# Optimization experiments

Hardware: AMD Instinct MI355X
Metric: run time of the kernel (lower is better)

Reference implementation:

```python
import jax, jax.numpy as jnp
import numpy as np

GRID = 64
N_NODES = GRID * GRID
LN_EPS = 1e-5


def _grid_edge_index(n=GRID):
    ids = np.arange(n * n, dtype=np.int32).reshape(n, n)
    r0, r1 = ids[:, :-1].ravel(), ids[:, 1:].ravel()   # horizontal neighbors
    d0, d1 = ids[:-1, :].ravel(), ids[1:, :].ravel()   # vertical neighbors
    src = np.concatenate([r0, r1, d0, d1])
    dst = np.concatenate([r1, r0, d1, d0])
    return np.stack([src, dst])  # [2, 16128] directed edges


def setup_inputs() -> dict:
    key = jax.random.key(0)
    ks = jax.random.split(key, 6)
    B, C, H, L = 128, 12, 64, 3
    s_in = 1.0 / np.sqrt(C)
    s_h = 1.0 / np.sqrt(H)
    return {
        "x": jax.random.normal(ks[0], (B, C, GRID, GRID), jnp.float32),
        "edge_index": jnp.asarray(_grid_edge_index()),
        "w_in": jax.random.normal(ks[1], (C, H), jnp.float32) * s_in,
        "b_in": jnp.zeros((H,), jnp.float32),
        "w_self": jax.random.normal(ks[2], (L, H, H), jnp.float32) * s_h,
        "w_neigh": jax.random.normal(ks[3], (L, H, H), jnp.float32) * s_h,
        "conv_b": jnp.zeros((L, H), jnp.float32),
        "ln_g": jnp.ones((L, H), jnp.float32),
        "ln_b": jnp.zeros((L, H), jnp.float32),
        "w_head": jax.random.normal(ks[4], (H, 1), jnp.float32) * s_h,
        "b_head": jnp.zeros((1,), jnp.float32),
    }


def reference(x, edge_index, w_in, b_in, w_self, w_neigh, conv_b, ln_g, ln_b, w_head, b_head):
    B = x.shape[0]
    BN = B * N_NODES
    # grid_to_nodes: [B, C, 64, 64] -> [B, N, C]
    nodes = jnp.transpose(x, (0, 2, 3, 1)).reshape(B, N_NODES, -1)
    h = (nodes @ w_in + b_in).reshape(BN, -1)
    # batched_edge_index: replicate with per-graph node offsets
    offs = (jnp.arange(B, dtype=edge_index.dtype) * N_NODES)
    ei = (edge_index[:, None, :] + offs[None, :, None]).reshape(2, -1)
    src, dst = ei[0], ei[1]
    deg = jax.ops.segment_sum(jnp.ones_like(src, dtype=h.dtype), dst, num_segments=BN)
    inv_deg = (1.0 / jnp.maximum(deg, 1.0))[:, None]
    n_layers = w_self.shape[0]
    for l in range(n_layers):
        # SAGE-mean conv: gather src feats, scatter-sum to dst, mean-normalize
        agg = jax.ops.segment_sum(h[src], dst, num_segments=BN) * inv_deg
        hn = h @ w_self[l] + agg @ w_neigh[l] + conv_b[l]
        mu = hn.mean(-1, keepdims=True)
        var = ((hn - mu) ** 2).mean(-1, keepdims=True)
        hn = (hn - mu) * jax.lax.rsqrt(var + LN_EPS) * ln_g[l] + ln_b[l]
        h = h + jax.nn.relu(hn)  # dropout is identity in eval mode
    logit = (h @ w_head + b_head).reshape(B, GRID, GRID)
    return logit
```

## Files before the change

kernel.cpp:

```cpp
#include <hip/hip_runtime.h>

#define GRID_D 64
#define NN (GRID_D * GRID_D)
#define H 64
#define C_IN 12
#define B_SZ 128
#define LN_EPS 1e-5f

typedef _Float16 f16x8 __attribute__((ext_vector_type(8)));
typedef _Float16 f16x4 __attribute__((ext_vector_type(4)));
typedef float    f32x4 __attribute__((ext_vector_type(4)));

#define AS1 __attribute__((address_space(1)))
#define AS3 __attribute__((address_space(3)))

__global__ __launch_bounds__(256) void k_inproj(
    const float* __restrict__ x, const float* __restrict__ w_in,
    const float* __restrict__ b_in, _Float16* __restrict__ h,
    const float* __restrict__ ws_, const float* __restrict__ wn_,
    _Float16* __restrict__ wt)
{
    int bid = blockIdx.x;
    int b = bid >> 6, r = bid & 63;
    int tid = threadIdx.x;

    int pi = bid * 256 + tid;
    if (pi < 3 * 2 * 4096) {
        int l = pi >> 13, g = (pi >> 12) & 1, j = (pi >> 6) & 63, k = pi & 63;
        const float* W = (g ? wn_ : ws_) + l * 4096;
        wt[pi] = (_Float16)W[k * 64 + j];
    }

    __shared__ float xs[C_IN][GRID_D];
    __shared__ float ws[C_IN][H];
    const float* xb = x + (size_t)b * C_IN * NN + (size_t)r * GRID_D;
    for (int idx = tid; idx < C_IN * GRID_D; idx += 256) {
        int c = idx >> 6, n = idx & 63;
        xs[c][n] = xb[(size_t)c * NN + n];
        ws[c][n] = w_in[idx];
    }
    __syncthreads();
    int n = tid >> 2;
    int j0 = (tid & 3) * 16;
    float acc[16];
    #pragma unroll
    for (int t = 0; t < 16; ++t) acc[t] = b_in[j0 + t];
    #pragma unroll
    for (int c = 0; c < C_IN; ++c) {
        float xv = xs[c][n];
        #pragma unroll
        for (int t = 0; t < 16; ++t) acc[t] += xv * ws[c][j0 + t];
    }
    _Float16* hp = h + (size_t)(b * NN + r * GRID_D + n) * H + j0;
    f16x8 o0, o1;
    #pragma unroll
    for (int t = 0; t < 8; ++t) { o0[t] = (_Float16)acc[t]; o1[t] = (_Float16)acc[8 + t]; }
    *(f16x8*)hp = o0;
    *(f16x8*)(hp + 8) = o1;
}

__device__ __forceinline__ void stage_row(
    const _Float16* hb, int grow, _Float16* slot, int wv, int ln)
{
    const _Float16* src = hb
        + (((size_t)(grow * GRID_D + wv * 8 + (ln >> 3))) << 6)
        + (((ln & 7) ^ (ln >> 3)) << 3);
    _Float16* dst = slot + wv * 512;
    __builtin_amdgcn_global_load_lds((const AS1 void*)src, (AS3 void*)dst, 16, 0, 0);
}

__global__ __launch_bounds__(768, 3) void k_fused(
    const _Float16* __restrict__ h0, float* __restrict__ logits,
    const _Float16* __restrict__ wtb,
    const float* __restrict__ cb, const float* __restrict__ lg,
    const float* __restrict__ lb,
    const float* __restrict__ w_head, const float* __restrict__ b_head)
{
    __shared__ _Float16 ring[3][4][4096];
    __shared__ _Float16 zbuf[4096];
    __shared__ float    pl[640];

    int tid = threadIdx.x, ln = tid & 63, wv = tid >> 6;
    int bid = blockIdx.x;
    int img = bid >> 1, chunk = bid & 1;
    int r0 = chunk << 5;
    const _Float16* hb = h0 + ((size_t)img << 18);

    int grp = wv >> 2;
    int ct  = wv & 3;
    int lrow = ln & 15, kgrp = ln >> 4;
    int col = ct * 16 + lrow;
    int cs = col & 7;
    int kq = kgrp * 4;
    bool cl = (col > 0), cr = (col < 63);

    const _Float16* wg = wtb + grp * 8192;
    f16x8 wsf[2][4], wnf[2][4];
    #pragma unroll
    for (int ks = 0; ks < 2; ++ks) {
        int k0 = ks * 32 + kq * 2;
        #pragma unroll
        for (int ft = 0; ft < 4; ++ft) {
            int j = ft * 16 + lrow;
            wsf[ks][ft] = *(const f16x8*)(wg + (j << 6) + k0);
            wnf[ks][ft] = *(const f16x8*)(wg + ((64 + j) << 6) + k0);
        }
    }
    #pragma unroll
    for (int ks = 0; ks < 2; ++ks)
        #pragma unroll
        for (int ft = 0; ft < 4; ++ft)
            asm volatile("" : "+v"(wsf[ks][ft]), "+v"(wnf[ks][ft]));

    if (tid < 576) {
        int l = tid / 192, r = tid % 192;
        pl[tid] = (r < 64) ? cb[l * 64 + r]
                : (r < 128) ? lg[l * 64 + r - 64] : lb[l * 64 + r - 128];
    } else if (tid < 640) {
        pl[tid] = w_head[tid - 576];
    }
    if (tid < 512) {
        f16x8 z = {};
        *(f16x8*)&zbuf[tid * 8] = z;
    }
    __syncthreads();

    const float* myp = pl + grp * 192;
    float bh = b_head[0];

    f32x4 cbq[4];
    #pragma unroll
    for (int ft = 0; ft < 4; ++ft) cbq[ft] = *(const f32x4*)&myp[ft * 16 + kq];

    int colo = col << 6;
    int cmo = cl ? (((col - 1) << 6)) : 0;
    int cpo = cr ? (((col + 1) << 6)) : 0;

    int lo0 = (r0 - 3 < 0) ? 0 : r0 - 3, hi0 = (r0 + 34 > 63) ? 63 : r0 + 34;
    int loC, hiC;
    if (grp == 0)      { loC = (r0 - 2 < 0) ? 0 : r0 - 2; hiC = (r0 + 33 > 63) ? 63 : r0 + 33; }
    else if (grp == 1) { loC = (r0 - 1 < 0) ? 0 : r0 - 1; hiC = (r0 + 32 > 63) ? 63 : r0 + 32; }
    else               { loC = r0;                         hiC = r0 + 31; }

    _Float16* rin  = &ring[grp][0][0];
    _Float16* rout = (grp < 2) ? &ring[grp + 1][0][0] : nullptr;

    #pragma unroll 1
    for (int s = 0; s <= 40; ++s) {
        int p0 = r0 - 3 + s;
        if (wv < 8 && p0 >= lo0 && p0 <= hi0)
            stage_row(hb, p0, &ring[0][p0 & 3][0], wv, ln);

        int pr = p0 - 2 * grp - 2;
        if (pr >= loC && pr <= hiC) {
            const _Float16* rc = rin + ((pr & 3) << 12);
            const _Float16* ruE = (pr > 0)  ? rin + (((pr - 1) & 3) << 12) : zbuf;
            const _Float16* rdE = (pr < 63) ? rin + (((pr + 1) & 3) << 12) : zbuf;
            _Float16 hinv = (_Float16)(1.0f / (float)((pr > 0) + (pr < 63) + cl + cr));

            f32x4 acc[4];
            #pragma unroll
            for (int ft = 0; ft < 4; ++ft) acc[ft] = (f32x4){0.f, 0.f, 0.f, 0.f};

            __builtin_amdgcn_s_setprio(1);
            #pragma unroll
            for (int ks = 0; ks < 2; ++ks) {
                int sl = ((ks * 4 + kgrp) ^ cs) << 3;
                f16x8 a = *(const f16x8*)(rc + colo + sl);
                #pragma unroll
                for (int ft = 0; ft < 4; ++ft)
                    acc[ft] = __builtin_amdgcn_mfma_f32_16x16x32_f16(wsf[ks][ft], a, acc[ft], 0, 0, 0);
            }

            #pragma unroll
            for (int ks = 0; ks < 2; ++ks) {
                int c8 = ks * 4 + kgrp;
                int sl = (c8 ^ cs) << 3;
                f16x8 u = *(const f16x8*)(ruE + colo + sl);
                f16x8 d = *(const f16x8*)(rdE + colo + sl);
                const _Float16* lp = cl ? (rc + cmo + ((c8 ^ ((col - 1) & 7)) << 3)) : zbuf;
                const _Float16* rp = cr ? (rc + cpo + ((c8 ^ ((col + 1) & 7)) << 3)) : zbuf;
                f16x8 lv = *(const f16x8*)lp;
                f16x8 rv = *(const f16x8*)rp;
                f16x8 sm = (lv + rv) + (u + d);
                f16x8 g;
                #pragma unroll
                for (int e = 0; e < 8; ++e) g[e] = sm[e] * hinv;
                #pragma unroll
                for (int ft = 0; ft < 4; ++ft)
                    acc[ft] = __builtin_amdgcn_mfma_f32_16x16x32_f16(wnf[ks][ft], g, acc[ft], 0, 0, 0);
            }
            __builtin_amdgcn_s_setprio(0);

            float s1 = 0.f, s2 = 0.f;
            #pragma unroll
            for (int ft = 0; ft < 4; ++ft) {
                acc[ft] += cbq[ft];
                #pragma unroll
                for (int t = 0; t < 4; ++t) { float xv = acc[ft][t]; s1 += xv; s2 += xv * xv; }
            }
            s1 += __shfl_xor(s1, 16); s1 += __shfl_xor(s1, 32);
            s2 += __shfl_xor(s2, 16); s2 += __shfl_xor(s2, 32);
            float mu   = s1 * (1.0f / H);
            float var  = s2 * (1.0f / H) - mu * mu;
            float rstd = rsqrtf(var + LN_EPS);

            const _Float16* res = rc + colo;
            if (grp < 2) {
                _Float16* outp = rout + ((pr & 3) << 12) + colo;
                #pragma unroll
                for (int ft = 0; ft < 4; ++ft) {
                    f32x4 lgq = *(const f32x4*)&myp[64 + ft * 16 + kq];
                    f32x4 lbq = *(const f32x4*)&myp[128 + ft * 16 + kq];
                    int slot = (ft * 2 + (kgrp >> 1)) ^ cs;
                    f16x4 rq = *(const f16x4*)(res + (slot << 3) + (kgrp & 1) * 4);
                    f16x4 oq;
                    #pragma unroll
                    for (int t = 0; t < 4; ++t) {
                        float o = (float)rq[t]
                                + fmaxf((acc[ft][t] - mu) * rstd * lgq[t] + lbq[t], 0.f);
                        oq[t] = (_Float16)o;
                    }
                    *(f16x4*)(outp + (slot << 3) + (kgrp & 1) * 4) = oq;
                }
            } else {
                float part = 0.f;
                #pragma unroll
                for (int ft = 0; ft < 4; ++ft) {
                    f32x4 lgq = *(const f32x4*)&myp[64 + ft * 16 + kq];
                    f32x4 lbq = *(const f32x4*)&myp[128 + ft * 16 + kq];
                    f32x4 whq = *(const f32x4*)&pl[576 + ft * 16 + kq];
                    int slot = (ft * 2 + (kgrp >> 1)) ^ cs;
                    f16x4 rq = *(const f16x4*)(res + (slot << 3) + (kgrp & 1) * 4);
                    #pragma unroll
                    for (int t = 0; t < 4; ++t) {
                        float o = (float)rq[t]
                                + fmaxf((acc[ft][t] - mu) * rstd * lgq[t] + lbq[t], 0.f);
                        part += o * whq[t];
                    }
                }
                part += __shfl_xor(part, 16);
                part += __shfl_xor(part, 32);
                if (kgrp == 0)
                    logits[(size_t)img * NN + pr * GRID_D + col] = part + bh;
            }
        }
        __syncthreads();
    }
}

extern "C" void kernel_launch(void* const* d_in, const int* in_sizes, int n_in,
                              void* d_out, int out_size, void* d_ws, size_t ws_size,
                              hipStream_t stream) {
    const float* x      = (const float*)d_in[0];
    const float* w_in   = (const float*)d_in[2];
    const float* b_in   = (const float*)d_in[3];
    const float* w_self = (const float*)d_in[4];
    const float* w_neigh= (const float*)d_in[5];
    const float* conv_b = (const float*)d_in[6];
    const float* ln_g   = (const float*)d_in[7];
    const float* ln_b   = (const float*)d_in[8];
    const float* w_head = (const float*)d_in[9];
    const float* b_head = (const float*)d_in[10];
    float* out = (float*)d_out;

    char* base = (char*)d_ws;
    const size_t HBYTES = (size_t)B_SZ * NN * H * sizeof(_Float16);
    _Float16* h_a = (_Float16*)base;
    _Float16* wtb = (_Float16*)(base + HBYTES);

    k_inproj<<<B_SZ * GRID_D, 256, 0, stream>>>(
        x, w_in, b_in, h_a, w_self, w_neigh, wtb);
    k_fused<<<B_SZ * 2, 768, 0, stream>>>(
        h_a, out, wtb, conv_b, ln_g, ln_b, w_head, b_head);
}
```

Baseline: 104.3 us.

## Use MFMA for input projection with larger per-block node tiles

Rewrites the input projection kernel to stage 256 nodes per block as fp16 in LDS (padded to K=32) and compute the 12->64 projection with 16x16x32 f16 MFMA instructions. Bias is added in fp32 before converting to fp16 and storing. The grid shrinks from 8192 to 2048 blocks, reducing launch and per-block overhead. Input is rounded to fp16 before the multiply, adding a small precision loss.

After: 104.5 us. No clear change (+0.2%).

```diff
diff --git a/kernel.cpp b/kernel.cpp
--- a/kernel.cpp
+++ b/kernel.cpp
@@ -20,8 +20,13 @@
     const float* __restrict__ ws_, const float* __restrict__ wn_,
     _Float16* __restrict__ wt)
 {
+    __shared__ _Float16 xs[256 * 40];
+    __shared__ _Float16 wl[64 * 40];
+    __shared__ float    bs[64];
+
     int bid = blockIdx.x;
-    int b = bid >> 6, r = bid & 63;
+    int img = bid >> 4, rq = bid & 15;
+    int base = rq * 256;
     int tid = threadIdx.x;
 
     int pi = bid * 256 + tid;
@@ -31,32 +36,69 @@
         wt[pi] = (_Float16)W[k * 64 + j];
     }
 
-    __shared__ float xs[C_IN][GRID_D];
-    __shared__ float ws[C_IN][H];
-    const float* xb = x + (size_t)b * C_IN * NN + (size_t)r * GRID_D;
-    for (int idx = tid; idx < C_IN * GRID_D; idx += 256) {
-        int c = idx >> 6, n = idx & 63;
-        xs[c][n] = xb[(size_t)c * NN + n];
-        ws[c][n] = w_in[idx];
+    {
+        const float* xg = x + (size_t)img * C_IN * NN + base;
+        int n = tid;
+        float xv[C_IN];
+        #pragma unroll
+        for (int c = 0; c < C_IN; ++c) xv[c] = xg[(size_t)c * NN + n];
+        f16x8 p0, p1, z = {};
+        #pragma unroll
+        for (int e = 0; e < 8; ++e) p0[e] = (_Float16)xv[e];
+        #pragma unroll
+        for (int e = 0; e < 4; ++e) p1[e] = (_Float16)xv[8 + e];
+        p1[4] = p1[5] = p1[6] = p1[7] = (_Float16)0.f;
+        _Float16* xd = xs + n * 40;
+        *(f16x8*)(xd)      = p0;
+        *(f16x8*)(xd + 8)  = p1;
+        *(f16x8*)(xd + 16) = z;
+        *(f16x8*)(xd + 24) = z;
+    }
+    {
+        int j = tid & 63, cg = tid >> 6;
+        #pragma unroll
+        for (int i = 0; i < 3; ++i) {
+            int c = cg * 3 + i;
+            wl[j * 40 + c] = (_Float16)w_in[c * 64 + j];
+        }
+        #pragma unroll
+        for (int i = 0; i < 5; ++i)
+            wl[j * 40 + 12 + cg * 5 + i] = (_Float16)0.f;
+        if (tid < 64) bs[tid] = b_in[tid];
     }
     __syncthreads();
-    int n = tid >> 2;
-    int j0 = (tid & 3) * 16;
-    float acc[16];
-    #pragma unroll
-    for (int t = 0; t < 16; ++t) acc[t] = b_in[j0 + t];
-    #pragma unroll
-    for (int c = 0; c < C_IN; ++c) {
-        float xv = xs[c][n];
-        #pragma unroll
-        for (int t = 0; t < 16; ++t) acc[t] += xv * ws[c][j0 + t];
-    }
-    _Float16* hp = h + (size_t)(b * NN + r * GRID_D + n) * H + j0;
-    f16x8 o0, o1;
-    #pragma unroll
-    for (int t = 0; t < 8; ++t) { o0[t] = (_Float16)acc[t]; o1[t] = (_Float16)acc[8 + t]; }
-    *(f16x8*)hp = o0;
-    *(f16x8*)(hp + 8) = o1;
+
+    int ln = tid & 63, wv = tid >> 6;
+    int lrow = ln & 15, kgrp = ln >> 4, kq = kgrp * 4;
+
+    f16x8 wf[4];
+    #pragma unroll
+    for (int ft = 0; ft < 4; ++ft)
+        wf[ft] = *(const f16x8*)(wl + (ft * 16 + lrow) * 40 + kgrp * 8);
+    f32x4 bq[4];
+    #pragma unroll
+    for (int ft = 0; ft < 4; ++ft) {
+        int j = ft * 16 + kq;
+        bq[ft] = (f32x4){bs[j], bs[j + 1], bs[j + 2], bs[j + 3]};
+    }
+
+    _Float16* hp = h + (((size_t)(img * NN + base + wv * 64)) << 6);
+    #pragma unroll
+    for (int nt = 0; nt < 4; ++nt) {
+        int node = wv * 64 + nt * 16 + lrow;
+        f16x8 a = *(const f16x8*)(xs + node * 40 + kgrp * 8);
+        f32x4 acc[4];
+        #pragma unroll
+        for (int ft = 0; ft < 4; ++ft) {
+            acc[ft] = __builtin_amdgcn_mfma_f32_16x16x32_f16(
+                wf[ft], a, (f32x4){0.f, 0.f, 0.f, 0.f}, 0, 0, 0);
+            acc[ft] += bq[ft];
+            f16x4 oq;
+            #pragma unroll
+            for (int t = 0; t < 4; ++t) oq[t] = (_Float16)acc[ft][t];
+            *(f16x4*)(hp + (((size_t)(nt * 16 + lrow)) << 6) + ft * 16 + kq) = oq;
+        }
+    }
 }
 
 __device__ __forceinline__ void stage_row(
@@ -269,7 +311,7 @@
     _Float16* h_a = (_Float16*)base;
     _Float16* wtb = (_Float16*)(base + HBYTES);
 
-    k_inproj<<<B_SZ * GRID_D, 256, 0, stream>>>(
+    k_inproj<<<B_SZ * 16, 256, 0, stream>>>(
         x, w_in, b_in, h_a, w_self, w_neigh, wtb);
     k_fused<<<B_SZ * 2, 768, 0, stream>>>(
         h_a, out, wtb, conv_b, ln_g, ln_b, w_head, b_head);
```
